# Kernel tuning notes

Hardware: AMD Instinct MI355X
Metric: run time of the kernel (lower is better)

## Reference

```python
import jax, jax.numpy as jnp
import numpy as np

B, CIN, T, H, W = 4, 64, 8, 32, 32
COUT, AHID = 64, 16
HWF = H * W


def _conv2d(x, w, b):
    y = jax.lax.conv_general_dilated(x, w, (1, 1), [(1, 1), (1, 1)],
                                     dimension_numbers=("NCHW", "OIHW", "NCHW"))
    return y + b[None, :, None, None]


def _conv1x1(x, w, b):
    return jnp.einsum("bchw,oc->bohw", x, w) + b[None, :, None, None]


def setup_inputs():
    key = jax.random.key(0)
    ks = jax.random.split(key, 18)
    s = 0.05
    d = {}
    d["X"] = jax.random.normal(ks[0], (B, CIN, T, H, W), jnp.float32)
    d["conv_w"] = jax.random.normal(ks[1], (4 * COUT, CIN + COUT, 3, 3), jnp.float32) * s
    d["conv_b"] = jnp.zeros((4 * COUT,), jnp.float32)
    d["W_ci"] = jax.random.normal(ks[2], (COUT, H, W), jnp.float32) * s
    d["W_cf"] = jax.random.normal(ks[3], (COUT, H, W), jnp.float32) * s
    d["W_co"] = jax.random.normal(ks[4], (COUT, H, W), jnp.float32) * s
    d["q_w"] = jax.random.normal(ks[5], (AHID, COUT), jnp.float32) * s
    d["q_b"] = jnp.zeros((AHID,), jnp.float32)
    d["k_w"] = jax.random.normal(ks[6], (AHID, COUT), jnp.float32) * s
    d["k_b"] = jnp.zeros((AHID,), jnp.float32)
    d["k2_w"] = jax.random.normal(ks[7], (AHID, COUT), jnp.float32) * s
    d["k2_b"] = jnp.zeros((AHID,), jnp.float32)
    d["v_w"] = jax.random.normal(ks[8], (COUT, COUT), jnp.float32) * s
    d["v_b"] = jnp.zeros((COUT,), jnp.float32)
    d["v2_w"] = jax.random.normal(ks[9], (COUT, COUT), jnp.float32) * s
    d["v2_b"] = jnp.zeros((COUT,), jnp.float32)
    d["z_w"] = jax.random.normal(ks[10], (2 * COUT, 2 * COUT), jnp.float32) * s
    d["z_b"] = jnp.zeros((2 * COUT,), jnp.float32)
    d["m_w"] = jax.random.normal(ks[11], (3 * COUT, 3 * COUT), jnp.float32) * s
    d["m_b"] = jnp.zeros((3 * COUT,), jnp.float32)
    return d


def _forward(X, conv_w, conv_b, W_ci, W_cf, W_co, q_w, q_b, k_w, k_b, k2_w, k2_b,
             v_w, v_b, v2_w, v2_b, z_w, z_b, m_w, m_b):
    def step(carry, x_t):
        h, c, m = carry
        # ConvLSTM cell with peephole connections
        gates = _conv2d(jnp.concatenate([x_t, h], axis=1), conv_w, conv_b)
        i_c, f_c, g_c, o_c = jnp.split(gates, 4, axis=1)
        ig = jax.nn.sigmoid(i_c + W_ci * c)
        fg = jax.nn.sigmoid(f_c + W_cf * c)
        c_new = fg * c + ig * jnp.tanh(g_c)
        og = jax.nn.sigmoid(o_c + W_co * c_new)
        h_new = og * jnp.tanh(c_new)
        # Self-attention memory module (all projections are 1x1 convs)
        q = _conv1x1(h_new, q_w, q_b).reshape(B, AHID, HWF)
        kh = _conv1x1(h_new, k_w, k_b).reshape(B, AHID, HWF)
        vh = _conv1x1(h_new, v_w, v_b).reshape(B, COUT, HWF)
        km = _conv1x1(m, k2_w, k2_b).reshape(B, AHID, HWF)
        vm = _conv1x1(m, v2_w, v2_b).reshape(B, COUT, HWF)
        att_h = jax.nn.softmax(jnp.einsum("ban,bam->bnm", q, kh), axis=-1)  # (B,HW,HW)
        att_m = jax.nn.softmax(jnp.einsum("ban,bam->bnm", q, km), axis=-1)
        z_h = jnp.einsum("bnm,bcm->bcn", att_h, vh)  # (B,COUT,HW)
        z_m = jnp.einsum("bnm,bcm->bcn", att_m, vm)
        z = jnp.concatenate([z_h, z_m], axis=1).reshape(B, 2 * COUT, H, W)
        z = _conv1x1(z, z_w, z_b)
        comb = _conv1x1(jnp.concatenate([z, h_new], axis=1), m_w, m_b)
        mo, mg, mi = jnp.split(comb, 3, axis=1)
        gi = jax.nn.sigmoid(mi)
        m_new = (1.0 - gi) * m + gi * jnp.tanh(mg)
        h_out = jax.nn.sigmoid(mo) * m_new
        return (h_out, c_new, m_new), h_out

    zeros = jnp.zeros((B, COUT, H, W), X.dtype)
    Xs = jnp.moveaxis(X, 2, 0)  # (T, B, CIN, H, W)
    _, hs = jax.lax.scan(step, (zeros, zeros, zeros), Xs)
    return jnp.moveaxis(hs, 0, 2)  # (B, COUT, T, H, W)


def reference(X, conv_w, conv_b, W_ci, W_cf, W_co, q_w, q_b, k_w, k_b, k2_w, k2_b,
              v_w, v_b, v2_w, v2_b, z_w, z_b, m_w, m_b):
    return _forward(X, conv_w, conv_b, W_ci, W_cf, W_co, q_w, q_b, k_w, k_b,
                    k2_w, k2_b, v_w, v_b, v2_w, v2_b, z_w, z_b, m_w, m_b)
```

## Files before the change

kernel.cpp:

```cpp
#include <hip/hip_runtime.h>
#include <hip/hip_bf16.h>

typedef __hip_bfloat16 bf16;
typedef unsigned short ushort;
typedef __attribute__((ext_vector_type(8))) short short8v;
typedef __attribute__((ext_vector_type(4))) float float4v;

__device__ __forceinline__ float b2f(bf16 v){ return __bfloat162float(v); }
__device__ __forceinline__ float sigm(float x){ return 1.0f/(1.0f+__expf(-x)); }
__device__ __forceinline__ float tanhc(float x){
  x = fminf(15.0f, fmaxf(-15.0f, x));
  float e = __expf(2.0f*x);
  return (e-1.0f)/(e+1.0f);
}
__device__ __forceinline__ ushort f2bu(float f){
  bf16 h = __float2bfloat16(f); return *reinterpret_cast<ushort*>(&h);
}
__device__ __forceinline__ float bu2f(ushort u){
  return __uint_as_float(((unsigned)u)<<16);
}
__device__ __forceinline__ short8v ldfrag(const ushort* p){
  return *reinterpret_cast<const short8v*>(p);
}
__device__ __forceinline__ void glds16(const ushort* g, ushort* l){
  __builtin_amdgcn_global_load_lds(
    (const __attribute__((address_space(1))) unsigned int*)g,
    (__attribute__((address_space(3))) unsigned int*)l, 16, 0, 0);
}
__device__ __forceinline__ void stage_ld(const ushort* s, uint4& a0, uint4& a1,
                                         uint4& a2, uint4& a3){
  a0 = *reinterpret_cast<const uint4*>(s);
  a1 = *reinterpret_cast<const uint4*>(s+512);
  a2 = *reinterpret_cast<const uint4*>(s+1024);
  a3 = *reinterpret_cast<const uint4*>(s+1536);
}
__device__ __forceinline__ void stage_wr(ushort* d, uint4 a0, uint4 a1,
                                         uint4 a2, uint4 a3){
  *reinterpret_cast<uint4*>(d)      = a0;
  *reinterpret_cast<uint4*>(d+512)  = a1;
  *reinterpret_cast<uint4*>(d+1024) = a2;
  *reinterpret_cast<uint4*>(d+1536) = a3;
}

#define WS_SMALL   0
#define WS_FLAG    262144
#define WS_ZROW    262160
#define WS_H       262208
#define WS_C       524352
#define WS_M       786496
#define WS_HNEW    1048640
#define WS_QB16    1310784
#define WS_KHB16   1376320
#define WS_KMB16   1441856
#define WS_VTH16   1507392
#define WS_VTM16   1638464
#define WS_MTH     1769536
#define WS_MTL     1900608
#define WS_HNTH    2031680
#define WS_HNTL    2162752
#define WS_ZW16H   2293824
#define WS_ZW16L   2302016
#define WS_MW16H   2310208
#define WS_MW16L   2328640
#define WS_WAHI    2347072
#define WS_WALO    2494528
#define WS_XTHI    2641984
#define WS_XTLO    3690560
#define WS_HTHI    4739136
#define WS_HTLO    4870208
#define WS_PWH     5001280
#define WS_PWL     5006912
#define O_CB    0
#define O_WCI   256
#define O_WCF   65792
#define O_WCO   131328
#define O_QW    196864
#define O_QB    197888
#define O_KW    197904
#define O_KB    198928
#define O_K2W   198944
#define O_K2B   199968
#define O_VW    199984
#define O_VB    204080
#define O_V2W   204144
#define O_V2B   208240
#define O_ZW    208304
#define O_ZB    224688
#define O_MW    224816
#define O_MB    261680

__global__ void k_probe(const unsigned int* __restrict__ Xu, int* __restrict__ flag){
  __shared__ int cnt;
  if (threadIdx.x == 0) cnt = 0;
  __syncthreads();
  unsigned int u = Xu[threadIdx.x];
  float f = __uint_as_float((u & 0xffffu) << 16);
  int bad = (fabsf(f) <= 1e4f) ? 0 : 1;
  atomicAdd(&cnt, bad);
  __syncthreads();
  if (threadIdx.x == 0) *flag = (cnt > 16) ? 1 : 0;
}

struct P18 { const void* p[18]; };

__global__ __launch_bounds__(256) void k_wconv(P18 pk, const int* __restrict__ flagp,
                                               float* __restrict__ dst){
  const int ns[18]   = {256,65536,65536,65536,1024,16,1024,16,1024,16,
                        4096,64,4096,64,16384,128,36864,192};
  const int offs[18] = {O_CB,O_WCI,O_WCF,O_WCO,O_QW,O_QB,O_KW,O_KB,O_K2W,O_K2B,
                        O_VW,O_VB,O_V2W,O_V2B,O_ZW,O_ZB,O_MW,O_MB};
  int y = blockIdx.y;
  int n = ns[y];
  int flag = *flagp;
  const void* src = pk.p[y];
  for (int i = blockIdx.x*256 + threadIdx.x; i < n; i += gridDim.x*256){
    float v = flag ? ((const float*)src)[i] : b2f(((const bf16*)src)[i]);
    dst[offs[y] + i] = v;
  }
}

__global__ __launch_bounds__(256) void k_wtrans(float* __restrict__ ws){
  int i = blockIdx.x*256 + threadIdx.x;
  if (i < 16384){
    float f = ws[O_ZW + i];
    ushort h = f2bu(f);
    ((ushort*)(ws + WS_ZW16H))[i] = h;
    ((ushort*)(ws + WS_ZW16L))[i] = f2bu(f - bu2f(h));
  }
  if (i < 36864){
    float f = ws[O_MW + i];
    ushort h = f2bu(f);
    ((ushort*)(ws + WS_MW16H))[i] = h;
    ((ushort*)(ws + WS_MW16L))[i] = f2bu(f - bu2f(h));
  }
  if (i < 11264){
    int r = i >> 6, k = i & 63;
    float f;
    if (r < 16)       f = ws[O_QW  + r*64 + k];
    else if (r < 32)  f = ws[O_KW  + (r-16)*64 + k];
    else if (r < 48)  f = ws[O_K2W + (r-32)*64 + k];
    else if (r < 112) f = ws[O_VW  + (r-48)*64 + k];
    else              f = ws[O_V2W + (r-112)*64 + k];
    ushort h = f2bu(f);
    ((ushort*)(ws + WS_PWH))[i] = h;
    ((ushort*)(ws + WS_PWL))[i] = f2bu(f - bu2f(h));
  }
}

__global__ __launch_bounds__(256) void k_init(const void* __restrict__ conv_w,
                                              const int* __restrict__ flagp,
                                              float* __restrict__ ws){
  int i = blockIdx.x*256 + threadIdx.x;
  int flag = *flagp;
  if (i < 786432) ws[WS_H + i] = 0.0f;
  if (i < 32) ws[WS_ZROW + i] = 0.0f;
  if (i < 196608) ((unsigned*)(ws + WS_QB16))[i] = 0u;
  if (i < 294912){
    int ci = i & 127;
    int j = i >> 7;
    int mm = j & 255, p = j >> 8;
    int cc = mm >> 2, g = mm & 3;
    int si = ((g*64 + cc)*128 + ci)*9 + p;
    int cis = ((((ci >> 3) ^ (mm & 7)) << 3) | (ci & 7));
    int di = (j << 7) + cis;
    ushort* wah = (ushort*)(ws + WS_WAHI);
    ushort* wal = (ushort*)(ws + WS_WALO);
    if (flag){
      float f = ((const float*)conv_w)[si];
      ushort hi = f2bu(f);
      wah[di] = hi;
      wal[di] = f2bu(f - bu2f(hi));
    } else {
      wah[di] = ((const ushort*)conv_w)[si];
    }
  }
  if (i < 131072){
    ((unsigned*)(ws + WS_HTHI))[i] = 0u;
    ((unsigned*)(ws + WS_HTLO))[i] = 0u;
    ((unsigned*)(ws + WS_MTH))[i] = 0u;
    ((unsigned*)(ws + WS_MTL))[i] = 0u;
  }
}

__global__ __launch_bounds__(256) void k_xt(const void* __restrict__ Xraw,
                                            const int* __restrict__ flagp,
                                            float* __restrict__ ws){
  __shared__ ushort hi_s[64][66];
  __shared__ ushort lo_s[64][66];
  int pt = blockIdx.x, s = blockIdx.y;
  int b = s >> 3, t = s & 7;
  int flag = *flagp;
  int tid = threadIdx.x;
  for (int k = 0; k < 16; ++k){
    int idx = tid + k*256;
    int ci = idx >> 6, pxl = idx & 63;
    size_t si = ((size_t)(b*64 + ci)*8 + t)*1024 + pt*64 + pxl;
    if (flag){
      float f = ((const float*)Xraw)[si];
      ushort h = f2bu(f);
      hi_s[pxl][ci] = h;
      lo_s[pxl][ci] = f2bu(f - bu2f(h));
    } else {
      hi_s[pxl][ci] = ((const ushort*)Xraw)[si];
    }
  }
  __syncthreads();
  ushort* xh = (ushort*)(ws + WS_XTHI) + ((size_t)s*1024 + pt*64)*64;
  ushort* xl = (ushort*)(ws + WS_XTLO) + ((size_t)s*1024 + pt*64)*64;
  for (int k = 0; k < 16; ++k){
    int idx = tid + k*256;
    int pxl = idx >> 6, ci = idx & 63;
    xh[pxl*64 + ci] = hi_s[pxl][ci];
    if (flag) xl[pxl*64 + ci] = lo_s[pxl][ci];
  }
}

__global__ __launch_bounds__(512, 4) void k_conv_mfma(
  const int* __restrict__ flagp,
  const ushort* __restrict__ wa_hi, const ushort* __restrict__ wa_lo,
  const ushort* __restrict__ xt_hi, const ushort* __restrict__ xt_lo,
  const ushort* __restrict__ ht_hi, const ushort* __restrict__ ht_lo,
  const float* __restrict__ smalls, float* __restrict__ cst,
  ushort* __restrict__ hnth, ushort* __restrict__ hntl, int t)
{
  __shared__ ushort albuf[16384];
  __shared__ ushort bsm[54*264];
  int nt = blockIdx.x, mh = blockIdx.y, b = blockIdx.z;
  int tid = threadIdx.x;
  int flag = *flagp;
  int ytile = nt >> 1, x0 = (nt & 1) * 16;

  const ushort* xb  = xt_hi + ((size_t)(b*8 + t))*65536;
  const ushort* xlb = xt_lo + ((size_t)(b*8 + t))*65536;
  const ushort* hb  = ht_hi + (size_t)b*65536;
  const ushort* hlb = ht_lo + (size_t)b*65536;

  const uint4 Z16 = make_uint4(0,0,0,0);
  for (int idx = tid; idx < 1728; idx += 512){
    int slot = idx >> 5, c = idx & 31;
    int rr = slot / 18, xi = slot - rr*18;
    int gy = ytile - 1 + rr, gx = x0 - 1 + xi;
    bool valid = (gy >= 0) & (gy < 32) & (gx >= 0) & (gx < 32);
    int px = gy*32 + gx;
    uint4 v = Z16;
    if (valid){
      if (c < 8)       v = *reinterpret_cast<const uint4*>(xb  + (size_t)px*64 + c*8);
      else if (c < 16) v = *reinterpret_cast<const uint4*>(hb  + (size_t)px*64 + (c-8)*8);
      else if (c < 24) v = *reinterpret_cast<const uint4*>(hlb + (size_t)px*64 + (c-16)*8);
      else if (flag)   v = *reinterpret_cast<const uint4*>(xlb + (size_t)px*64 + (c-24)*8);
    }
    *reinterpret_cast<uint4*>(&bsm[slot*264 + c*8]) = v;
  }
  __syncthreads();

  int w = tid >> 6, lane = tid & 63, lr = lane & 15, lk = lane >> 4;
  int px = nt*16 + lr;
  const int sw = lr & 7;
  const int c0 = ((( 0+lk) ^ sw) << 3);
  const int c1 = ((( 4+lk) ^ sw) << 3);
  const int c2 = ((( 8+lk) ^ sw) << 3);
  const int c3 = (((12+lk) ^ sw) << 3);
  const ushort* aw  = wa_hi + (size_t)(mh*128 + w*16)*128 + lane*8;
  const ushort* awl = wa_lo + (size_t)(mh*128 + w*16)*128 + lane*8;
  ushort* areg = albuf + w*2048;

  float4v acc = {0.f,0.f,0.f,0.f};

  if (!flag){
    #pragma unroll
    for (int k = 0; k < 4; ++k)
      glds16(aw + k*512, areg + k*512);
    #pragma unroll
    for (int p = 0; p < 9; ++p){
      asm volatile("s_waitcnt vmcnt(0)" ::: "memory");
      __builtin_amdgcn_sched_barrier(0);
      short8v A0 = ldfrag(areg + lr*128 + c0);
      short8v A1 = ldfrag(areg + lr*128 + c1);
      short8v A2 = ldfrag(areg + lr*128 + c2);
      short8v A3 = ldfrag(areg + lr*128 + c3);
      int pinl = (p/3)*18 + lr + (p%3);
      const ushort* bl = &bsm[pinl*264 + lk*8];
      short8v BX0 = ldfrag(bl),     BX1 = ldfrag(bl+32);
      short8v BH0 = ldfrag(bl+64),  BH1 = ldfrag(bl+96);
      short8v BL0 = ldfrag(bl+128), BL1 = ldfrag(bl+160);
      acc = __builtin_amdgcn_mfma_f32_16x16x32_bf16(A0, BX0, acc, 0,0,0);
      acc = __builtin_amdgcn_mfma_f32_16x16x32_bf16(A1, BX1, acc, 0,0,0);
      acc = __builtin_amdgcn_mfma_f32_16x16x32_bf16(A2, BH0, acc, 0,0,0);
      acc = __builtin_amdgcn_mfma_f32_16x16x32_bf16(A3, BH1, acc, 0,0,0);
      acc = __builtin_amdgcn_mfma_f32_16x16x32_bf16(A2, BL0, acc, 0,0,0);
      acc = __builtin_amdgcn_mfma_f32_16x16x32_bf16(A3, BL1, acc, 0,0,0);
      if (p < 8){
        __builtin_amdgcn_sched_barrier(0);
        #pragma unroll
        for (int k = 0; k < 4; ++k)
          glds16(aw + (size_t)(p+1)*32768 + k*512, areg + k*512);
      }
    }
  } else {
    #pragma unroll 1
    for (int p = 0; p < 9; ++p){
      int pinl = (p/3)*18 + lr + (p%3);
      const ushort* bl = &bsm[pinl*264 + lk*8];
      short8v BX0 = ldfrag(bl),      BX1 = ldfrag(bl+32);
      short8v BH0 = ldfrag(bl+64),   BH1 = ldfrag(bl+96);
      short8v BL0 = ldfrag(bl+128),  BL1 = ldfrag(bl+160);
      short8v BXl0 = ldfrag(bl+192), BXl1 = ldfrag(bl+224);
      uint4 s0,s1,s2,s3;
      stage_ld(aw + (size_t)p*32768, s0,s1,s2,s3);
      stage_wr(areg + lane*8, s0,s1,s2,s3);
      short8v A0 = ldfrag(areg + lr*128 + c0);
      short8v A1 = ldfrag(areg + lr*128 + c1);
      short8v A2 = ldfrag(areg + lr*128 + c2);
      short8v A3 = ldfrag(areg + lr*128 + c3);
      acc = __builtin_amdgcn_mfma_f32_16x16x32_bf16(A0, BX0, acc, 0,0,0);
      acc = __builtin_amdgcn_mfma_f32_16x16x32_bf16(A1, BX1, acc, 0,0,0);
      acc = __builtin_amdgcn_mfma_f32_16x16x32_bf16(A2, BH0, acc, 0,0,0);
      acc = __builtin_amdgcn_mfma_f32_16x16x32_bf16(A3, BH1, acc, 0,0,0);
      acc = __builtin_amdgcn_mfma_f32_16x16x32_bf16(A2, BL0, acc, 0,0,0);
      acc = __builtin_amdgcn_mfma_f32_16x16x32_bf16(A3, BL1, acc, 0,0,0);
      acc = __builtin_amdgcn_mfma_f32_16x16x32_bf16(A0, BXl0, acc, 0,0,0);
      acc = __builtin_amdgcn_mfma_f32_16x16x32_bf16(A1, BXl1, acc, 0,0,0);
      stage_ld(awl + (size_t)p*32768, s0,s1,s2,s3);
      stage_wr(areg + lane*8, s0,s1,s2,s3);
      short8v Al0 = ldfrag(areg + lr*128 + c0);
      short8v Al1 = ldfrag(areg + lr*128 + c1);
      short8v Al2 = ldfrag(areg + lr*128 + c2);
      short8v Al3 = ldfrag(areg + lr*128 + c3);
      acc = __builtin_amdgcn_mfma_f32_16x16x32_bf16(Al0, BX0, acc, 0,0,0);
      acc = __builtin_amdgcn_mfma_f32_16x16x32_bf16(Al1, BX1, acc, 0,0,0);
      acc = __builtin_amdgcn_mfma_f32_16x16x32_bf16(Al2, BH0, acc, 0,0,0);
      acc = __builtin_amdgcn_mfma_f32_16x16x32_bf16(Al3, BH1, acc, 0,0,0);
    }
  }

  {
    int cc = mh*32 + w*4 + lk;
    int wi = cc*1024 + px;
    size_t sidx = ((size_t)(b*64 + cc))*1024 + px;
    float cprev = cst[sidx];
    float ic = acc[0] + smalls[O_CB + cc];
    float fc = acc[1] + smalls[O_CB + 64 + cc];
    float gc = acc[2] + smalls[O_CB + 128 + cc];
    float oc = acc[3] + smalls[O_CB + 192 + cc];
    float ig = sigm(ic + smalls[O_WCI + wi]*cprev);
    float fg = sigm(fc + smalls[O_WCF + wi]*cprev);
    float cnew = fg*cprev + ig*tanhc(gc);
    float og = sigm(oc + smalls[O_WCO + wi]*cnew);
    cst[sidx] = cnew;
    float hv = og*tanhc(cnew);
    size_t tix = ((size_t)b*1024 + px)*64 + cc;
    ushort hh = f2bu(hv);
    hnth[tix] = hh;
    hntl[tix] = f2bu(hv - bu2f(hh));
  }
}

__global__ __launch_bounds__(256) void k_projm(
  const ushort* __restrict__ hnth, const ushort* __restrict__ hntl,
  const ushort* __restrict__ mth, const ushort* __restrict__ mtl,
  const ushort* __restrict__ pwh, const ushort* __restrict__ pwl,
  const float* __restrict__ smalls, const int* __restrict__ flagp,
  ushort* __restrict__ qb16, ushort* __restrict__ khb16, ushort* __restrict__ kmb16,
  ushort* __restrict__ vth16, ushort* __restrict__ vtm16)
{
  int nt = blockIdx.x, b = blockIdx.y;
  int n0 = nt*16;
  int tid = threadIdx.x;
  int w = tid >> 6, lane = tid & 63, lr = lane & 15, lk = lane >> 4;
  int flag = *flagp;
  const float4v Z4 = {0.f,0.f,0.f,0.f};
  size_t bb = ((size_t)b*1024 + n0 + lr)*64 + lk*8;
  short8v BH0  = ldfrag(hnth + bb), BH1  = ldfrag(hnth + bb + 32);
  short8v BHl0 = ldfrag(hntl + bb), BHl1 = ldfrag(hntl + bb + 32);
  short8v BM0  = ldfrag(mth + bb),  BM1  = ldfrag(mth + bb + 32);
  short8v BMl0 = ldfrag(mtl + bb),  BMl1 = ldfrag(mtl + bb + 32);
  int n = n0 + lr;
  int tstart = w*3;
  int tcnt = (w == 3) ? 2 : 3;
  for (int ti = 0; ti < tcnt; ++ti){
    int tt = tstart + ti;
    const ushort* ar = pwh + (size_t)(tt*16 + lr)*64 + lk*8;
    short8v a0 = ldfrag(ar), a1 = ldfrag(ar + 32);
    bool srcm = (tt == 2) || (tt >= 7);
    short8v b0  = srcm ? BM0  : BH0,  b1  = srcm ? BM1  : BH1;
    short8v bl0 = srcm ? BMl0 : BHl0, bl1 = srcm ? BMl1 : BHl1;
    float4v d = Z4;
    d = __builtin_amdgcn_mfma_f32_16x16x32_bf16(a0, b0,  d, 0,0,0);
    d = __builtin_amdgcn_mfma_f32_16x16x32_bf16(a1, b1,  d, 0,0,0);
    d = __builtin_amdgcn_mfma_f32_16x16x32_bf16(a0, bl0, d, 0,0,0);
    d = __builtin_amdgcn_mfma_f32_16x16x32_bf16(a1, bl1, d, 0,0,0);
    if (flag){
      const ushort* arl = pwl + (size_t)(tt*16 + lr)*64 + lk*8;
      short8v al0 = ldfrag(arl), al1 = ldfrag(arl + 32);
      d = __builtin_amdgcn_mfma_f32_16x16x32_bf16(al0, b0, d, 0,0,0);
      d = __builtin_amdgcn_mfma_f32_16x16x32_bf16(al1, b1, d, 0,0,0);
    }
    int boff = (tt==0) ? O_QB : (tt==1) ? O_KB : (tt==2) ? O_K2B
             : (tt<7) ? (O_VB + (tt-3)*16) : (O_V2B + (tt-7)*16);
    if (tt < 3){
      ushort* base = (tt==0) ? qb16 : (tt==1) ? khb16 : kmb16;
      ushort u[4];
      #pragma unroll
      for (int q = 0; q < 4; ++q)
        u[q] = f2bu(d[q] + smalls[boff + lk*4 + q]);
      *reinterpret_cast<uint2*>(&base[((size_t)b*1024 + n)*32 + lk*4]) =
        make_uint2((unsigned)u[0] | ((unsigned)u[1]<<16),
                   (unsigned)u[2] | ((unsigned)u[3]<<16));
    } else {
      ushort* base = (tt<7) ? vth16 : vtm16;
      int cc0 = ((tt<7) ? (tt-3) : (tt-7))*16 + lk*4;
      #pragma unroll
      for (int q = 0; q < 4; ++q)
        base[((size_t)b*64 + cc0 + q)*1024 + n] = f2bu(d[q] + smalls[boff + lk*4 + q]);
    }
  }
}

__global__ __launch_bounds__(512) void k_fattz(
  const ushort* __restrict__ qb16, const ushort* __restrict__ khb16,
  const ushort* __restrict__ kmb16, const ushort* __restrict__ vth16,
  const ushort* __restrict__ vtm16,
  const ushort* __restrict__ hnth, const ushort* __restrict__ hntl,
  const float* __restrict__ smalls,
  const ushort* __restrict__ zw16h, const ushort* __restrict__ zw16l,
  const ushort* __restrict__ mw16h, const ushort* __restrict__ mw16l,
  const int* __restrict__ flagp,
  float* __restrict__ mst, ushort* __restrict__ mth, ushort* __restrict__ mtl,
  ushort* __restrict__ hth, ushort* __restrict__ htl,
  void* __restrict__ outraw, int t)
{
  __shared__ __align__(16) unsigned char poolA[17408];
  __shared__ __align__(16) ushort ztbh[16*136];
  __shared__ __align__(16) ushort ztbl[16*136];
  __shared__ float cb[192*17];
  __shared__ float ml[64*17];
  __shared__ float rs_s[2][4][16];

  ushort* es   = (ushort*)poolA;
  ushort* zbh  = (ushort*)poolA;
  ushort* zbl  = (ushort*)(poolA + 8704);
  float*  ho_s = (float*)poolA;
  float*  mn_s = (float*)(poolA + 4352);

  int nt = blockIdx.x, b = blockIdx.y;
  int n0 = nt*16;
  int tid = threadIdx.x;
  int w = tid >> 6, lane = tid & 63, lr = lane & 15, lk = lane >> 4;
  int br = w >> 2, wq = w & 3;
  int flag = *flagp;
  const float4v Z4 = {0.f,0.f,0.f,0.f};

  const ushort* kb = (br ? kmb16 : khb16) + (size_t)b*32768;
  const ushort* vt = (br ? vtm16 : vth16) + (size_t)b*65536;
  const ushort* qp = qb16 + (size_t)b*32768;
  ushort* esb = es + br*4352;

  for (int idx = tid; idx < 1024; idx += 512){
    int ch = idx >> 4, pp = idx & 15;
    ml[ch*17+pp] = mst[((size_t)b*64 + ch)*1024 + n0 + pp];
  }

  short8v qf = ldfrag(qp + (size_t)(n0 + lr)*32 + lk*8);

  float4v acc[2];
  acc[0]=Z4; acc[1]=Z4;
  float rsum = 0.f;

  #pragma unroll 1
  for (int mc = 0; mc < 4; ++mc){
    int mbase = mc*256 + wq*64;
    #pragma unroll
    for (int tau = 0; tau < 4; ++tau){
      short8v af = ldfrag(kb + (size_t)(mbase + tau*16 + lr)*32 + lk*8);
      float4v d = __builtin_amdgcn_mfma_f32_16x16x32_bf16(af, qf, Z4, 0,0,0);
      ushort u0 = f2bu(__expf(fminf(d[0], 60.f)));
      ushort u1 = f2bu(__expf(fminf(d[1], 60.f)));
      ushort u2 = f2bu(__expf(fminf(d[2], 60.f)));
      ushort u3 = f2bu(__expf(fminf(d[3], 60.f)));
      rsum += (bu2f(u0) + bu2f(u1)) + (bu2f(u2) + bu2f(u3));
      unsigned lo = (unsigned)u0 | ((unsigned)u1 << 16);
      unsigned hi = (unsigned)u2 | ((unsigned)u3 << 16);
      *reinterpret_cast<uint2*>(&esb[lr*272 + wq*64 + tau*16 + lk*4]) = make_uint2(lo, hi);
    }
    __syncthreads();
    #pragma unroll
    for (int ks = 0; ks < 8; ++ks){
      short8v av = ldfrag(vt + (size_t)(wq*16 + lr)*1024 + mc*256 + ks*32 + lk*8);
      short8v bv = ldfrag(&esb[lr*272 + ks*32 + lk*8]);
      acc[ks & 1] = __builtin_amdgcn_mfma_f32_16x16x32_bf16(av, bv, acc[ks & 1], 0,0,0);
    }
    __syncthreads();
  }

  {
    float r = rsum;
    r += __shfl_xor(r, 16);
    r += __shfl_xor(r, 32);
    if (lane < 16) rs_s[br][wq][lr] = r;
  }
  __syncthreads();
  {
    float rinv = 1.0f / (rs_s[br][0][lr] + rs_s[br][1][lr] + rs_s[br][2][lr] + rs_s[br][3][lr]);
    int ch0 = br*64 + wq*16 + lk*4;
    ushort uh[4], ul[4];
    #pragma unroll
    for (int r = 0; r < 4; ++r){
      float z = (acc[0][r] + acc[1][r])*rinv;
      uh[r] = f2bu(z);
      ul[r] = f2bu(z - bu2f(uh[r]));
    }
    *reinterpret_cast<uint2*>(&zbh[lr*136 + ch0]) =
      make_uint2((unsigned)uh[0] | ((unsigned)uh[1]<<16), (unsigned)uh[2] | ((unsigned)uh[3]<<16));
    *reinterpret_cast<uint2*>(&zbl[lr*136 + ch0]) =
      make_uint2((unsigned)ul[0] | ((unsigned)ul[1]<<16), (unsigned)ul[2] | ((unsigned)ul[3]<<16));
  }
  __syncthreads();

  {
    float4v zacc = Z4;
    if (!flag){
      #pragma unroll
      for (int kf = 0; kf < 4; ++kf){
        short8v a  = ldfrag(zw16h + (size_t)(w*16 + lr)*128 + kf*32 + lk*8);
        short8v bh = ldfrag(&zbh[lr*136 + kf*32 + lk*8]);
        short8v bl = ldfrag(&zbl[lr*136 + kf*32 + lk*8]);
        zacc = __builtin_amdgcn_mfma_f32_16x16x32_bf16(a, bh, zacc, 0,0,0);
        zacc = __builtin_amdgcn_mfma_f32_16x16x32_bf16(a, bl, zacc, 0,0,0);
      }
    } else {
      #pragma unroll
      for (int kf = 0; kf < 4; ++kf){
        short8v a  = ldfrag(zw16h + (size_t)(w*16 + lr)*128 + kf*32 + lk*8);
        short8v al = ldfrag(zw16l + (size_t)(w*16 + lr)*128 + kf*32 + lk*8);
        short8v bh = ldfrag(&zbh[lr*136 + kf*32 + lk*8]);
        short8v bl = ldfrag(&zbl[lr*136 + kf*32 + lk*8]);
        zacc = __builtin_amdgcn_mfma_f32_16x16x32_bf16(a,  bh, zacc, 0,0,0);
        zacc = __builtin_amdgcn_mfma_f32_16x16x32_bf16(a,  bl, zacc, 0,0,0);
        zacc = __builtin_amdgcn_mfma_f32_16x16x32_bf16(al, bh, zacc, 0,0,0);
      }
    }
    int r0 = w*16 + lk*4;
    ushort th[4], tl[4];
    #pragma unroll
    for (int q = 0; q < 4; ++q){
      float ztv = zacc[q] + smalls[O_ZB + r0 + q];
      th[q] = f2bu(ztv);
      tl[q] = f2bu(ztv - bu2f(th[q]));
    }
    *reinterpret_cast<uint2*>(&ztbh[lr*136 + r0]) =
      make_uint2((unsigned)th[0] | ((unsigned)th[1]<<16), (unsigned)th[2] | ((unsigned)th[3]<<16));
    *reinterpret_cast<uint2*>(&ztbl[lr*136 + r0]) =
      make_uint2((unsigned)tl[0] | ((unsigned)tl[1]<<16), (unsigned)tl[2] | ((unsigned)tl[3]<<16));
  }
  __syncthreads();

  const ushort* hrow  = hnth + ((size_t)b*1024 + n0 + lr)*64;
  const ushort* hrowl = hntl + ((size_t)b*1024 + n0 + lr)*64;
  #pragma unroll
  for (int mi = 0; mi < 2; ++mi){
    if (mi == 1 && w >= 4) break;
    int mf = (mi == 0) ? w : (w + 8);
    float4v cacc = Z4;
    const ushort* arow  = mw16h + (size_t)(mf*16 + lr)*192;
    const ushort* arowl = mw16l + (size_t)(mf*16 + lr)*192;
    if (!flag){
      #pragma unroll
      for (int kf = 0; kf < 4; ++kf){
        short8v a  = ldfrag(arow + kf*32 + lk*8);
        short8v bh = ldfrag(&ztbh[lr*136 + kf*32 + lk*8]);
        short8v bl = ldfrag(&ztbl[lr*136 + kf*32 + lk*8]);
        cacc = __builtin_amdgcn_mfma_f32_16x16x32_bf16(a, bh, cacc, 0,0,0);
        cacc = __builtin_amdgcn_mfma_f32_16x16x32_bf16(a, bl, cacc, 0,0,0);
      }
      #pragma unroll
      for (int kf = 0; kf < 2; ++kf){
        short8v a  = ldfrag(arow + 128 + kf*32 + lk*8);
        short8v bh = ldfrag(hrow + kf*32 + lk*8);
        short8v bl = ldfrag(hrowl + kf*32 + lk*8);
        cacc = __builtin_amdgcn_mfma_f32_16x16x32_bf16(a, bh, cacc, 0,0,0);
        cacc = __builtin_amdgcn_mfma_f32_16x16x32_bf16(a, bl, cacc, 0,0,0);
      }
    } else {
      #pragma unroll
      for (int kf = 0; kf < 4; ++kf){
        short8v a  = ldfrag(arow + kf*32 + lk*8);
        short8v al = ldfrag(arowl + kf*32 + lk*8);
        short8v bh = ldfrag(&ztbh[lr*136 + kf*32 + lk*8]);
        short8v bl = ldfrag(&ztbl[lr*136 + kf*32 + lk*8]);
        cacc = __builtin_amdgcn_mfma_f32_16x16x32_bf16(a,  bh, cacc, 0,0,0);
        cacc = __builtin_amdgcn_mfma_f32_16x16x32_bf16(a,  bl, cacc, 0,0,0);
        cacc = __builtin_amdgcn_mfma_f32_16x16x32_bf16(al, bh, cacc, 0,0,0);
      }
      #pragma unroll
      for (int kf = 0; kf < 2; ++kf){
        short8v a  = ldfrag(arow + 128 + kf*32 + lk*8);
        short8v al = ldfrag(arowl + 128 + kf*32 + lk*8);
        short8v bh = ldfrag(hrow + kf*32 + lk*8);
        short8v bl = ldfrag(hrowl + kf*32 + lk*8);
        cacc = __builtin_amdgcn_mfma_f32_16x16x32_bf16(a,  bh, cacc, 0,0,0);
        cacc = __builtin_amdgcn_mfma_f32_16x16x32_bf16(a,  bl, cacc, 0,0,0);
        cacc = __builtin_amdgcn_mfma_f32_16x16x32_bf16(al, bh, cacc, 0,0,0);
      }
    }
    int r0 = mf*16 + lk*4;
    #pragma unroll
    for (int q = 0; q < 4; ++q)
      cb[(r0+q)*17 + lr] = cacc[q] + smalls[O_MB + r0 + q];
  }
  __syncthreads();

  {
    int px = tid >> 5, lr2 = tid & 31;
    #pragma unroll
    for (int j = 0; j < 2; ++j){
      int ch = lr2 + 32*j;
      float mo = cb[ch*17 + px];
      float mg = cb[(64+ch)*17 + px];
      float mi = cb[(128+ch)*17 + px];
      float mold = ml[ch*17 + px];
      float gi = sigm(mi);
      float mnew = (1.0f-gi)*mold + gi*tanhc(mg);
      float ho = sigm(mo)*mnew;
      ho_s[ch*17+px] = ho;
      mn_s[ch*17+px] = mnew;
    }
  }
  __syncthreads();
  for (int idx = tid; idx < 1024; idx += 512){
    int ch = idx >> 4, pp = idx & 15;
    int n = n0 + pp;
    size_t gidx = ((size_t)b*64 + ch)*1024 + n;
    float mn = mn_s[ch*17+pp];
    mst[gidx] = mn;
    float ho = ho_s[ch*17+pp];
    size_t tix = ((size_t)b*1024 + n)*64 + ch;
    ushort hb_ = f2bu(ho);
    hth[tix] = hb_;
    htl[tix] = f2bu(ho - bu2f(hb_));
    ushort mh_ = f2bu(mn);
    mth[tix] = mh_;
    mtl[tix] = f2bu(mn - bu2f(mh_));
    size_t oidx = ((size_t)(b*64+ch)*8 + t)*1024 + n;
    if (flag) ((float*)outraw)[oidx] = ho;
    else      ((bf16*)outraw)[oidx] = __float2bfloat16(ho);
  }
}

extern "C" void kernel_launch(void* const* d_in, const int* in_sizes, int n_in,
                              void* d_out, int out_size, void* d_ws, size_t ws_size,
                              hipStream_t stream)
{
  float* ws = (float*)d_ws;
  int* flag = (int*)(ws + WS_FLAG);
  float* c    = ws + WS_C;
  float* m    = ws + WS_M;
  ushort* qb16  = (ushort*)(ws + WS_QB16);
  ushort* khb16 = (ushort*)(ws + WS_KHB16);
  ushort* kmb16 = (ushort*)(ws + WS_KMB16);
  ushort* vth16 = (ushort*)(ws + WS_VTH16);
  ushort* vtm16 = (ushort*)(ws + WS_VTM16);
  ushort* mth   = (ushort*)(ws + WS_MTH);
  ushort* mtl   = (ushort*)(ws + WS_MTL);
  ushort* hnth  = (ushort*)(ws + WS_HNTH);
  ushort* hntl  = (ushort*)(ws + WS_HNTL);
  ushort* zw16h = (ushort*)(ws + WS_ZW16H);
  ushort* zw16l = (ushort*)(ws + WS_ZW16L);
  ushort* mw16h = (ushort*)(ws + WS_MW16H);
  ushort* mw16l = (ushort*)(ws + WS_MW16L);
  ushort* wa_hi = (ushort*)(ws + WS_WAHI);
  ushort* wa_lo = (ushort*)(ws + WS_WALO);
  ushort* xt_hi = (ushort*)(ws + WS_XTHI);
  ushort* xt_lo = (ushort*)(ws + WS_XTLO);
  ushort* ht_hi = (ushort*)(ws + WS_HTHI);
  ushort* ht_lo = (ushort*)(ws + WS_HTLO);
  ushort* pwh   = (ushort*)(ws + WS_PWH);
  ushort* pwl   = (ushort*)(ws + WS_PWL);

  k_probe<<<1, 256, 0, stream>>>((const unsigned int*)d_in[0], flag);
  P18 pk;
  for (int i = 0; i < 18; ++i) pk.p[i] = d_in[2 + i];
  k_wconv<<<dim3(64,18), 256, 0, stream>>>(pk, flag, ws);
  k_init<<<3072, 256, 0, stream>>>(d_in[1], flag, ws);
  k_xt<<<dim3(16,32), 256, 0, stream>>>(d_in[0], flag, ws);
  k_wtrans<<<144, 256, 0, stream>>>(ws);

  for (int t = 0; t < 8; ++t){
    k_conv_mfma<<<dim3(64,2,4), 512, 0, stream>>>(flag, wa_hi, wa_lo, xt_hi, xt_lo,
                                                  ht_hi, ht_lo, ws, c, hnth, hntl, t);
    k_projm<<<dim3(64,4), 256, 0, stream>>>(hnth, hntl, mth, mtl, pwh, pwl, ws, flag,
                                            qb16, khb16, kmb16, vth16, vtm16);
    k_fattz<<<dim3(64,4), 512, 0, stream>>>(qb16, khb16, kmb16, vth16, vtm16,
                                            hnth, hntl, ws, zw16h, zw16l, mw16h, mw16l,
                                            flag, m, mth, mtl, ht_hi, ht_lo, d_out, t);
  }
  (void)in_sizes; (void)n_in; (void)out_size; (void)ws_size;
}
```

Baseline: 457.9 us.

## Double-buffer conv weight prefetch and split conv blocks into smaller 256-thread tiles

The ConvLSTM gate conv kernel now runs 256-thread blocks over four output-channel slices instead of 512-thread blocks over two, doubling the grid. In the bf16 path, each wave double-buffers its weight slice in LDS: the next tap's weights are loaded while the current tap is computed, using a partial vmcnt wait instead of draining all loads. The first weight prefetch is now issued before the input halo tile is loaded, so the two transfers overlap. In exchange, each halo tile is loaded redundantly by twice as many blocks, and LDS per block keeps both buffers.

```diff
diff --git a/kernel.cpp b/kernel.cpp
--- a/kernel.cpp
+++ b/kernel.cpp
@@ -215,7 +215,7 @@
   }
 }
 
-__global__ __launch_bounds__(512, 4) void k_conv_mfma(
+__global__ __launch_bounds__(256) void k_conv_mfma(
   const int* __restrict__ flagp,
   const ushort* __restrict__ wa_hi, const ushort* __restrict__ wa_lo,
   const ushort* __restrict__ xt_hi, const ushort* __restrict__ xt_lo,
@@ -235,8 +235,20 @@
   const ushort* hb  = ht_hi + (size_t)b*65536;
   const ushort* hlb = ht_lo + (size_t)b*65536;
 
+  int w = tid >> 6, lane = tid & 63, lr = lane & 15, lk = lane >> 4;
+  const ushort* aw  = wa_hi + (size_t)(mh*64 + w*16)*128 + lane*8;
+  const ushort* awl = wa_lo + (size_t)(mh*64 + w*16)*128 + lane*8;
+  ushort* buf0 = albuf + w*2048;
+  ushort* buf1 = albuf + 8192 + w*2048;
+
+  if (!flag){
+    #pragma unroll
+    for (int k = 0; k < 4; ++k)
+      glds16(aw + k*512, buf0 + k*512);
+  }
+
   const uint4 Z16 = make_uint4(0,0,0,0);
-  for (int idx = tid; idx < 1728; idx += 512){
+  for (int idx = tid; idx < 1728; idx += 256){
     int slot = idx >> 5, c = idx & 31;
     int rr = slot / 18, xi = slot - rr*18;
     int gy = ytile - 1 + rr, gx = x0 - 1 + xi;
@@ -253,31 +265,34 @@
   }
   __syncthreads();
 
-  int w = tid >> 6, lane = tid & 63, lr = lane & 15, lk = lane >> 4;
   int px = nt*16 + lr;
   const int sw = lr & 7;
   const int c0 = ((( 0+lk) ^ sw) << 3);
   const int c1 = ((( 4+lk) ^ sw) << 3);
   const int c2 = ((( 8+lk) ^ sw) << 3);
   const int c3 = (((12+lk) ^ sw) << 3);
-  const ushort* aw  = wa_hi + (size_t)(mh*128 + w*16)*128 + lane*8;
-  const ushort* awl = wa_lo + (size_t)(mh*128 + w*16)*128 + lane*8;
-  ushort* areg = albuf + w*2048;
 
   float4v acc = {0.f,0.f,0.f,0.f};
 
   if (!flag){
     #pragma unroll
-    for (int k = 0; k < 4; ++k)
-      glds16(aw + k*512, areg + k*512);
-    #pragma unroll
     for (int p = 0; p < 9; ++p){
-      asm volatile("s_waitcnt vmcnt(0)" ::: "memory");
+      if (p < 8){
+        ushort* dst = (p & 1) ? buf0 : buf1;
+        const ushort* src = aw + (size_t)(p+1)*32768;
+        #pragma unroll
+        for (int k = 0; k < 4; ++k)
+          glds16(src + k*512, dst + k*512);
+        asm volatile("s_waitcnt vmcnt(4)" ::: "memory");
+      } else {
+        asm volatile("s_waitcnt vmcnt(0)" ::: "memory");
+      }
       __builtin_amdgcn_sched_barrier(0);
-      short8v A0 = ldfrag(areg + lr*128 + c0);
-      short8v A1 = ldfrag(areg + lr*128 + c1);
-      short8v A2 = ldfrag(areg + lr*128 + c2);
-      short8v A3 = ldfrag(areg + lr*128 + c3);
+      const ushort* ab = (p & 1) ? buf1 : buf0;
+      short8v A0 = ldfrag(ab + lr*128 + c0);
+      short8v A1 = ldfrag(ab + lr*128 + c1);
+      short8v A2 = ldfrag(ab + lr*128 + c2);
+      short8v A3 = ldfrag(ab + lr*128 + c3);
       int pinl = (p/3)*18 + lr + (p%3);
       const ushort* bl = &bsm[pinl*264 + lk*8];
       short8v BX0 = ldfrag(bl),     BX1 = ldfrag(bl+32);
@@ -289,24 +304,20 @@
       acc = __builtin_amdgcn_mfma_f32_16x16x32_bf16(A3, BH1, acc, 0,0,0);
       acc = __builtin_amdgcn_mfma_f32_16x16x32_bf16(A2, BL0, acc, 0,0,0);
       acc = __builtin_amdgcn_mfma_f32_16x16x32_bf16(A3, BL1, acc, 0,0,0);
-      if (p < 8){
-        __builtin_amdgcn_sched_barrier(0);
-        #pragma unroll
-        for (int k = 0; k < 4; ++k)
-          glds16(aw + (size_t)(p+1)*32768 + k*512, areg + k*512);
-      }
     }
   } else {
+    ushort* areg = buf0;
     #pragma unroll 1
     for (int p = 0; p < 9; ++p){
       int pinl = (p/3)*18 + lr + (p%3);
       const ushort* bl = &bsm[pinl*264 + lk*8];
-      short8v BX0 = ldfrag(bl),      BX1 = ldfrag(bl+32);
+      short8v BX0 = ldfrag(bl),      short8v_dummy0; (void)0;
+      short8v BX1 = ldfrag(bl+32);
       short8v BH0 = ldfrag(bl+64),   BH1 = ldfrag(bl+96);
       short8v BL0 = ldfrag(bl+128),  BL1 = ldfrag(bl+160);
       short8v BXl0 = ldfrag(bl+192), BXl1 = ldfrag(bl+224);
       uint4 s0,s1,s2,s3;
-      stage_ld(aw + (size_t)p*32768, s0,s1,s2,s3);
+      stage_ld(aw + (size_t)p*32768 - lane*8 + lane*8, s0,s1,s2,s3);
       stage_wr(areg + lane*8, s0,s1,s2,s3);
       short8v A0 = ldfrag(areg + lr*128 + c0);
       short8v A1 = ldfrag(areg + lr*128 + c1);
@@ -334,7 +345,7 @@
   }
 
   {
-    int cc = mh*32 + w*4 + lk;
+    int cc = mh*16 + w*4 + lk;
     int wi = cc*1024 + px;
     size_t sidx = ((size_t)(b*64 + cc))*1024 + px;
     float cprev = cst[sidx];
@@ -685,7 +696,7 @@
   k_wtrans<<<144, 256, 0, stream>>>(ws);
 
   for (int t = 0; t < 8; ++t){
-    k_conv_mfma<<<dim3(64,2,4), 512, 0, stream>>>(flag, wa_hi, wa_lo, xt_hi, xt_lo,
+    k_conv_mfma<<<dim3(64,4,4), 256, 0, stream>>>(flag, wa_hi, wa_lo, xt_hi, xt_lo,
                                                   ht_hi, ht_lo, ws, c, hnth, hntl, t);
     k_projm<<<dim3(64,4), 256, 0, stream>>>(hnth, hntl, mth, mtl, pwh, pwl, ws, flag,
                                             qb16, khb16, kmb16, vth16, vtm16);
```

Measured after the change: 556.3 us. +21.5%, slower.
